# Optimization experiments

Hardware: AMD Instinct MI355X
Metric: run time of the kernel (lower is better)

The kernel has to match this reference:

```python
import jax, jax.numpy as jnp
import numpy as np


def _elem_mlp(x, w1, b1, w2, b2):
    # elementwise 1 -> N -> 1 ReLU MLP (distilled exp / inv approximators)
    h = jax.nn.relu(x[..., None] * w1[:, 0] + b1)  # [..., N]
    return jnp.einsum('...n,n->...', h, w2[0]) + b2[0]


def setup_inputs() -> dict:
    key = jax.random.key(0)
    ks = jax.random.split(key, 13)
    T, S, B, D = 8, 512, 8, 512
    NE, NI = 32, 64
    f = jnp.float32
    inp = {
        'sx': jax.random.normal(ks[0], (T, S, B, D), f) * 0.1,
        'q_proj_weight': jax.random.normal(ks[1], (D, D), f) / np.sqrt(D),
        'k_proj_weight': jax.random.normal(ks[2], (D, D), f) / np.sqrt(D),
        'q_proj_bias': jax.random.normal(ks[3], (D,), f) * 0.02,
        'k_proj_bias': jax.random.normal(ks[4], (D,), f) * 0.02,
        'exp_w1': jax.random.normal(ks[5], (NE, 1), f),
        'exp_b1': jax.random.normal(ks[6], (NE,), f) * 0.1,
        'exp_w2': jax.random.normal(ks[7], (1, NE), f) / np.sqrt(NE),
        'exp_b2': jax.random.normal(ks[8], (1,), f) * 0.01,
        'inv_w1': jax.random.normal(ks[9], (NI, 1), f),
        'inv_b1': jax.random.normal(ks[10], (NI,), f) * 0.1,
        'inv_w2': jax.random.normal(ks[11], (1, NI), f) / np.sqrt(NI),
        'inv_b2': jax.random.normal(ks[12], (1,), f) * 0.01,
        'num_heads': 8,
    }
    return inp


def reference(sx, q_proj_weight, k_proj_weight, q_proj_bias, k_proj_bias,
              exp_w1, exp_b1, exp_w2, exp_b2,
              inv_w1, inv_b1, inv_w2, inv_b2, num_heads):
    T, S, B, D = sx.shape
    H = num_heads
    hd = D // H
    scale = 1.0 / np.sqrt(hd)

    def proj(x_t, W, b):
        # [S, B, D] -> [B*H, S, hd]
        y = x_t @ W.T + b
        return y.reshape(S, B * H, hd).transpose(1, 0, 2)

    def step(carry, x_t):
        sum_q, sum_k, sum_p = carry
        sq = proj(x_t, q_proj_weight, q_proj_bias)
        sk = proj(x_t, k_proj_weight, k_proj_bias)
        sum_q = sum_q + sq
        # sp_t = sum_q @ sk^T + sq @ sum_k^T (sum_k updated AFTER, per snn_qk_product)
        sp = (jnp.einsum('bsh,bth->bst', sum_q, sk)
              + jnp.einsum('bsh,bth->bst', sq, sum_k)) * scale
        sum_k = sum_k + sk
        return (sum_q, sum_k, sum_p + sp), None

    z_qk = jnp.zeros((B * H, S, hd), sx.dtype)
    z_p = jnp.zeros((B * H, S, S), sx.dtype)
    (sum_q, sum_k, sum_p), _ = jax.lax.scan(step, (z_qk, z_qk, z_p), sx)

    p = sum_p / T  # time-averaged accumulated QK product

    # fit_softmax: distilled-MLP softmax approximation
    tmax = p[:, :, 0:1]
    tp = jnp.minimum(p - (tmax - 1.0), 3.0)
    x_up = jnp.where(tp > -20.0,
                     _elem_mlp(tp, exp_w1, exp_b1, exp_w2, exp_b2), 0.0)
    partition = x_up.sum(-1, keepdims=True)
    p_inv = _elem_mlp(partition, inv_w1, inv_b1, inv_w2, inv_b2)
    out = x_up * p_inv
    partition_p2 = out.sum(-1, keepdims=True)
    p_inv2 = _elem_mlp(partition_p2, inv_w1, inv_b1, inv_w2, inv_b2)
    out2 = jnp.where(partition_p2 > 1.5, out * p_inv2, out)
    return out2
```

## Files before the change

### kernel.cpp

```cpp
#include <hip/hip_runtime.h>


#define T_  8
#define NE_ 32
#define NI_ 64

#define LUT_N   4096
#define LUT_LO  -20.0f
#define LUT_HI  3.0f
#define LUT_INVW (LUT_N / (LUT_HI - LUT_LO))
#define LUT_W    ((LUT_HI - LUT_LO) / LUT_N)

typedef __attribute__((ext_vector_type(8))) short bf16x8;
typedef __attribute__((ext_vector_type(4))) float f32x4;

#define XS_OFF 0u
#define WQ_OFF 2097152u
#define WK_OFF 2359296u
#define QB_OFF 2621440u
#define KB_OFF 4718592u
#define LUT_OFF 6815744u

__device__ inline unsigned short f2bf(float f) {
  union { float f; unsigned u; } v; v.f = f;
  unsigned r = v.u + 0x7FFFu + ((v.u >> 16) & 1u);
  return (unsigned short)(r >> 16);
}

__device__ inline void gload16(const void* g, void* l) {
  __builtin_amdgcn_global_load_lds(
      (const __attribute__((address_space(1))) void*)g,
      (__attribute__((address_space(3))) void*)l, 16, 0, 0);
}

__device__ inline bf16x8 lds_read_swz(const unsigned short* base, int row, int byteoff) {
  int addr = row * 128 + (byteoff ^ ((row & 7) << 4));
  return *(const bf16x8*)((const char*)base + addr);
}

__device__ inline float invmlp(float x, const float* __restrict__ w1,
                               const float* __restrict__ b1,
                               const float* __restrict__ w2, float b2) {
  float a = b2;
#pragma unroll 8
  for (int n = 0; n < NI_; n++) a += w2[n] * fmaxf(x * w1[n] + b1[n], 0.0f);
  return a;
}

__device__ inline float expmlp_exact(float t, const float* __restrict__ w1,
                                     const float* __restrict__ b1,
                                     const float* __restrict__ w2, float b2) {
  float a = b2;
#pragma unroll
  for (int n = 0; n < NE_; n++) a += w2[n] * fmaxf(t * w1[n] + b1[n], 0.0f);
  return a;
}

__global__ __launch_bounds__(256) void k_pre(
    const float* __restrict__ sx, const float* __restrict__ wq,
    const float* __restrict__ wk, const float* __restrict__ ew1,
    const float* __restrict__ eb1, const float* __restrict__ ew2,
    const float* __restrict__ eb2p,
    unsigned short* __restrict__ xs, unsigned short* __restrict__ wqb,
    unsigned short* __restrict__ wkb, float2* __restrict__ lut) {
  int bx = blockIdx.x, tid = threadIdx.x;
  if (bx < 2048) {
    size_t i = ((size_t)bx * 256 + tid) * 4;
    float4 a = *(const float4*)(sx + i);
#pragma unroll
    for (int t = 1; t < T_; t++) {
      float4 v = *(const float4*)(sx + (size_t)t * 2097152 + i);
      a.x += v.x; a.y += v.y; a.z += v.z; a.w += v.w;
    }
    ushort4 o; o.x = f2bf(a.x); o.y = f2bf(a.y); o.z = f2bf(a.z); o.w = f2bf(a.w);
    *(ushort4*)(xs + i) = o;
  } else if (bx < 2560) {
    const float* src = (bx < 2304) ? wq : wk;
    unsigned short* dst = (bx < 2304) ? wqb : wkb;
    int base = (bx < 2304) ? 2048 : 2304;
    size_t i = ((size_t)(bx - base) * 256 + tid) * 4;
    float4 a = *(const float4*)(src + i);
    ushort4 o; o.x = f2bf(a.x); o.y = f2bf(a.y); o.z = f2bf(a.z); o.w = f2bf(a.w);
    *(ushort4*)(dst + i) = o;
  } else {
    int i = (bx - 2560) * 256 + tid;
    float b2 = eb2p[0];
    float tl = fmaf((float)i, LUT_W, LUT_LO);
    float th = fmaf((float)(i + 1), LUT_W, LUT_LO);
    float el = expmlp_exact(tl, ew1, eb1, ew2, b2);
    float eh = expmlp_exact(th, ew1, eb1, ew2, b2);
    float alpha = (eh - el) * LUT_INVW;
    float beta = fmaf(-alpha, tl, el);
    lut[i] = make_float2(alpha, beta);
  }
}

__global__ __launch_bounds__(256, 2) void k_proj(
    const unsigned short* __restrict__ xs, const unsigned short* __restrict__ wb,
    const float* __restrict__ bq, const float* __restrict__ bk,
    unsigned short* __restrict__ outb) {
  __shared__ unsigned short As[128 * 64];
  __shared__ unsigned short Bs[128 * 64];
  int tid = threadIdx.x;
  int lane = tid & 63, w = tid >> 6;
  int r0 = blockIdx.x * 128;
  int c0 = blockIdx.y * 128;
  int z = blockIdx.z;
  const unsigned short* W = wb + (size_t)z * 262144;
  const float* bias = z ? bk : bq;
  unsigned short* dst = outb + (size_t)z * 2097152;
  float sc = z ? 1.0f : (1.0f / 64.0f);

  int rgrp = lane >> 4, cl = lane & 15;
  int r0w = (w >> 1) * 64, c0w = (w & 1) * 64;

  f32x4 acc[4][4];
  f32x4 zero = {0.f, 0.f, 0.f, 0.f};
#pragma unroll
  for (int m = 0; m < 4; m++)
#pragma unroll
    for (int n = 0; n < 4; n++) acc[m][n] = zero;

  int rl = lane >> 3, slot = lane & 7;

  for (int kt = 0; kt < 8; kt++) {
    int k0 = kt * 64;
#pragma unroll
    for (int i = 0; i < 4; i++) {
      int chunk = w * 4 + i;
      int r = chunk * 8 + rl;
      int sw = (slot ^ (r & 7)) * 8;
      gload16(xs + (size_t)(r0 + r) * 512 + k0 + sw, (char*)As + chunk * 1024);
      gload16(W + (size_t)(c0 + r) * 512 + k0 + sw, (char*)Bs + chunk * 1024);
    }
    __syncthreads();
#pragma unroll
    for (int kb = 0; kb < 2; kb++) {
      bf16x8 af[4], bfr[4];
#pragma unroll
      for (int m = 0; m < 4; m++) af[m] = lds_read_swz(As, r0w + 16 * m + cl, kb * 64 + rgrp * 16);
#pragma unroll
      for (int n = 0; n < 4; n++) bfr[n] = lds_read_swz(Bs, c0w + 16 * n + cl, kb * 64 + rgrp * 16);
#pragma unroll
      for (int m = 0; m < 4; m++)
#pragma unroll
        for (int n = 0; n < 4; n++)
          acc[m][n] = __builtin_amdgcn_mfma_f32_16x16x32_bf16(af[m], bfr[n], acc[m][n], 0, 0, 0);
    }
    __syncthreads();
  }

#pragma unroll
  for (int n = 0; n < 4; n++) {
    int cg = c0 + c0w + 16 * n + cl;
    float bv = 8.0f * bias[cg];
    int h = cg >> 6, dh = cg & 63;
    int chunk = dh >> 3, hh = chunk >> 2, rg2 = chunk & 3, jj = dh & 7;
#pragma unroll
    for (int m = 0; m < 4; m++) {
#pragma unroll
      for (int j = 0; j < 4; j++) {
        int rg = r0 + r0w + 16 * m + rgrp * 4 + j;
        int s = rg >> 3, b = rg & 7;
        int bh = b * 8 + h;
        int cb = s >> 4, cls = s & 15;
        size_t idx = ((size_t)((bh * 32 + cb) * 2 + hh)) * 512 + (rg2 * 16 + cls) * 8 + jj;
        dst[idx] = f2bf((acc[m][n][j] + bv) * sc);
      }
    }
  }
}

__global__ __launch_bounds__(256, 4) void k_attn(
    const unsigned short* __restrict__ qb, const unsigned short* __restrict__ kb,
    const float2* __restrict__ lutg,
    const float* __restrict__ iw1, const float* __restrict__ ib1,
    const float* __restrict__ iw2, const float* __restrict__ ib2p,
    float* __restrict__ out) {
  __shared__ float2 Lut[LUT_N];
  __shared__ float s_part[4][16];
  __shared__ float s_fac[16];

  int tid = threadIdx.x;
  int lane = tid & 63, w = tid >> 6;
  int i = blockIdx.x;
  int xcd = i & 7, j2 = i >> 3;
  int bh = xcd * 8 + (j2 >> 5);
  int rb = j2 & 31;
  int rgrp = lane >> 4, cl = lane & 15;

#pragma unroll
  for (int c = 0; c < 8; c++) {
    int chunk = w * 8 + c;
    gload16((const char*)lutg + chunk * 1024 + lane * 16, (char*)Lut + chunk * 1024);
  }

  const char* Qb = (const char*)qb + (size_t)((bh * 32 + rb) * 2) * 1024;
  bf16x8 aF0 = *(const bf16x8*)(Qb + lane * 16);
  bf16x8 aF1 = *(const bf16x8*)(Qb + 1024 + lane * 16);

  const char* Kbase = (const char*)kb + (size_t)(bh * 32) * 2048;
  f32x4 zero = {0.f, 0.f, 0.f, 0.f};

  float tm1[4];
  {
    bf16x8 b0 = *(const bf16x8*)(Kbase + lane * 16);
    bf16x8 b1 = *(const bf16x8*)(Kbase + 1024 + lane * 16);
    f32x4 p0 = __builtin_amdgcn_mfma_f32_16x16x32_bf16(aF0, b0, zero, 0, 0, 0);
    p0 = __builtin_amdgcn_mfma_f32_16x16x32_bf16(aF1, b1, p0, 0, 0, 0);
    int src = lane & 48;
#pragma unroll
    for (int j = 0; j < 4; j++) tm1[j] = __shfl(p0[j], src) - 1.0f;
  }

  f32x4 acc[8];
#pragma unroll
  for (int f = 0; f < 8; f++) {
    const char* Kb = Kbase + (size_t)(w * 8 + f) * 2048;
    bf16x8 b0 = *(const bf16x8*)(Kb + lane * 16);
    bf16x8 b1 = *(const bf16x8*)(Kb + 1024 + lane * 16);
    acc[f] = __builtin_amdgcn_mfma_f32_16x16x32_bf16(aF0, b0, zero, 0, 0, 0);
    acc[f] = __builtin_amdgcn_mfma_f32_16x16x32_bf16(aF1, b1, acc[f], 0, 0, 0);
  }

  __syncthreads();

  const float C0 = -LUT_LO * LUT_INVW;
  float rowsum[4] = {0.f, 0.f, 0.f, 0.f};
#pragma unroll
  for (int f = 0; f < 8; f++) {
#pragma unroll
    for (int j = 0; j < 4; j++) {
      float tp = fminf(acc[f][j] - tm1[j], 3.0f);
      float u = fmaf(tp, LUT_INVW, C0);
      u = fminf(fmaxf(u, 0.0f), (float)(LUT_N - 1));
      float2 ab = Lut[(int)u];
      float xu = fmaf(ab.x, tp, ab.y);
      xu = (tp > -20.0f) ? xu : 0.0f;
      acc[f][j] = xu;
      rowsum[j] += xu;
    }
  }

#pragma unroll
  for (int j = 0; j < 4; j++) {
    float s = rowsum[j];
    s += __shfl_xor(s, 1);
    s += __shfl_xor(s, 2);
    s += __shfl_xor(s, 4);
    s += __shfl_xor(s, 8);
    if (cl == 0) s_part[w][rgrp * 4 + j] = s;
  }
  __syncthreads();

  if (tid < 16) {
    float part = s_part[0][tid] + s_part[1][tid] + s_part[2][tid] + s_part[3][tid];
    float pinv = invmlp(part, iw1, ib1, iw2, ib2p[0]);
    float pp2 = part * pinv;
    float fac = pinv;
    if (pp2 > 1.5f) fac *= invmlp(pp2, iw1, ib1, iw2, ib2p[0]);
    s_fac[tid] = fac;
  }
  __syncthreads();

  float* outb = out + ((size_t)bh * 512 + rb * 16) * 512;
#pragma unroll
  for (int j = 0; j < 4; j++) {
    int row = rgrp * 4 + j;
    float fac = s_fac[row];
#pragma unroll
    for (int f = 0; f < 8; f++)
      __builtin_nontemporal_store(acc[f][j] * fac,
          &outb[(size_t)row * 512 + w * 128 + 16 * f + cl]);
  }
}

extern "C" void kernel_launch(void* const* d_in, const int* in_sizes, int n_in,
                              void* d_out, int out_size, void* d_ws, size_t ws_size,
                              hipStream_t stream) {
  (void)in_sizes; (void)n_in; (void)out_size; (void)ws_size;
  const float* sx  = (const float*)d_in[0];
  const float* wq  = (const float*)d_in[1];
  const float* wk  = (const float*)d_in[2];
  const float* bq  = (const float*)d_in[3];
  const float* bk  = (const float*)d_in[4];
  const float* ew1 = (const float*)d_in[5];
  const float* eb1 = (const float*)d_in[6];
  const float* ew2 = (const float*)d_in[7];
  const float* eb2 = (const float*)d_in[8];
  const float* iw1 = (const float*)d_in[9];
  const float* ib1 = (const float*)d_in[10];
  const float* iw2 = (const float*)d_in[11];
  const float* ib2 = (const float*)d_in[12];
  unsigned short* wsu = (unsigned short*)d_ws;
  float2* lut = (float2*)(wsu + LUT_OFF);
  float* out = (float*)d_out;

  k_pre<<<2576, 256, 0, stream>>>(sx, wq, wk, ew1, eb1, ew2, eb2,
                                  wsu + XS_OFF, wsu + WQ_OFF, wsu + WK_OFF, lut);
  k_proj<<<dim3(32, 4, 2), 256, 0, stream>>>(wsu + XS_OFF, wsu + WQ_OFF, bq, bk, wsu + QB_OFF);
  k_attn<<<2048, 256, 0, stream>>>(wsu + QB_OFF, wsu + KB_OFF, lut,
                                   iw1, ib1, iw2, ib2, out);
}
```

Measured before the change: 55.47 us.

## Stage projection output in LDS, shrink LUT to values, parallelize inverse MLP

The projection epilogue now writes its bf16 results into shared memory and then emits coalesced 16-byte stores, replacing scattered 2-byte global stores. The exp lookup table stores one value per point instead of an (alpha, beta) pair and interpolates between neighbours, which halves its shared memory footprint and allows occupancy 5 for the attention kernel. The inverse MLP is now computed redundantly by every lane with four accumulators and broadcast by shuffle, which removes a barrier and the single-wavefront serial section. The input time-sum uses nontemporal loads. Costs are two LDS reads per lookup and duplicated MLP work on every lane.

```diff
diff --git a/kernel.cpp b/kernel.cpp
--- a/kernel.cpp
+++ b/kernel.cpp
@@ -13,6 +13,7 @@
 
 typedef __attribute__((ext_vector_type(8))) short bf16x8;
 typedef __attribute__((ext_vector_type(4))) float f32x4;
+typedef __attribute__((ext_vector_type(4))) unsigned int u32x4;
 
 #define XS_OFF 0u
 #define WQ_OFF 2097152u
@@ -38,13 +39,18 @@
   return *(const bf16x8*)((const char*)base + addr);
 }
 
-__device__ inline float invmlp(float x, const float* __restrict__ w1,
-                               const float* __restrict__ b1,
-                               const float* __restrict__ w2, float b2) {
-  float a = b2;
-#pragma unroll 8
-  for (int n = 0; n < NI_; n++) a += w2[n] * fmaxf(x * w1[n] + b1[n], 0.0f);
-  return a;
+__device__ inline float invmlp4(float x, const float* __restrict__ w1,
+                                const float* __restrict__ b1,
+                                const float* __restrict__ w2, float b2) {
+  float a0 = b2, a1 = 0.f, a2 = 0.f, a3 = 0.f;
+#pragma unroll
+  for (int n = 0; n < NI_; n += 4) {
+    a0 += w2[n + 0] * fmaxf(x * w1[n + 0] + b1[n + 0], 0.0f);
+    a1 += w2[n + 1] * fmaxf(x * w1[n + 1] + b1[n + 1], 0.0f);
+    a2 += w2[n + 2] * fmaxf(x * w1[n + 2] + b1[n + 2], 0.0f);
+    a3 += w2[n + 3] * fmaxf(x * w1[n + 3] + b1[n + 3], 0.0f);
+  }
+  return (a0 + a1) + (a2 + a3);
 }
 
 __device__ inline float expmlp_exact(float t, const float* __restrict__ w1,
@@ -62,17 +68,17 @@
     const float* __restrict__ eb1, const float* __restrict__ ew2,
     const float* __restrict__ eb2p,
     unsigned short* __restrict__ xs, unsigned short* __restrict__ wqb,
-    unsigned short* __restrict__ wkb, float2* __restrict__ lut) {
+    unsigned short* __restrict__ wkb, float* __restrict__ lut) {
   int bx = blockIdx.x, tid = threadIdx.x;
   if (bx < 2048) {
     size_t i = ((size_t)bx * 256 + tid) * 4;
-    float4 a = *(const float4*)(sx + i);
+    f32x4 a = __builtin_nontemporal_load((const f32x4*)(sx + i));
 #pragma unroll
     for (int t = 1; t < T_; t++) {
-      float4 v = *(const float4*)(sx + (size_t)t * 2097152 + i);
-      a.x += v.x; a.y += v.y; a.z += v.z; a.w += v.w;
-    }
-    ushort4 o; o.x = f2bf(a.x); o.y = f2bf(a.y); o.z = f2bf(a.z); o.w = f2bf(a.w);
+      f32x4 v = __builtin_nontemporal_load((const f32x4*)(sx + (size_t)t * 2097152 + i));
+      a += v;
+    }
+    ushort4 o; o.x = f2bf(a[0]); o.y = f2bf(a[1]); o.z = f2bf(a[2]); o.w = f2bf(a[3]);
     *(ushort4*)(xs + i) = o;
   } else if (bx < 2560) {
     const float* src = (bx < 2304) ? wq : wk;
@@ -84,14 +90,10 @@
     *(ushort4*)(dst + i) = o;
   } else {
     int i = (bx - 2560) * 256 + tid;
-    float b2 = eb2p[0];
-    float tl = fmaf((float)i, LUT_W, LUT_LO);
-    float th = fmaf((float)(i + 1), LUT_W, LUT_LO);
-    float el = expmlp_exact(tl, ew1, eb1, ew2, b2);
-    float eh = expmlp_exact(th, ew1, eb1, ew2, b2);
-    float alpha = (eh - el) * LUT_INVW;
-    float beta = fmaf(-alpha, tl, el);
-    lut[i] = make_float2(alpha, beta);
+    if (i <= LUT_N) {
+      float t = fmaf((float)i, LUT_W, LUT_LO);
+      lut[i] = expmlp_exact(t, ew1, eb1, ew2, eb2p[0]);
+    }
   }
 }
 
@@ -99,8 +101,7 @@
     const unsigned short* __restrict__ xs, const unsigned short* __restrict__ wb,
     const float* __restrict__ bq, const float* __restrict__ bk,
     unsigned short* __restrict__ outb) {
-  __shared__ unsigned short As[128 * 64];
-  __shared__ unsigned short Bs[128 * 64];
+  __shared__ unsigned short Sh[2][128 * 64];
   int tid = threadIdx.x;
   int lane = tid & 63, w = tid >> 6;
   int r0 = blockIdx.x * 128;
@@ -130,17 +131,17 @@
       int chunk = w * 4 + i;
       int r = chunk * 8 + rl;
       int sw = (slot ^ (r & 7)) * 8;
-      gload16(xs + (size_t)(r0 + r) * 512 + k0 + sw, (char*)As + chunk * 1024);
-      gload16(W + (size_t)(c0 + r) * 512 + k0 + sw, (char*)Bs + chunk * 1024);
+      gload16(xs + (size_t)(r0 + r) * 512 + k0 + sw, (char*)Sh[0] + chunk * 1024);
+      gload16(W + (size_t)(c0 + r) * 512 + k0 + sw, (char*)Sh[1] + chunk * 1024);
     }
     __syncthreads();
 #pragma unroll
     for (int kb = 0; kb < 2; kb++) {
       bf16x8 af[4], bfr[4];
 #pragma unroll
-      for (int m = 0; m < 4; m++) af[m] = lds_read_swz(As, r0w + 16 * m + cl, kb * 64 + rgrp * 16);
-#pragma unroll
-      for (int n = 0; n < 4; n++) bfr[n] = lds_read_swz(Bs, c0w + 16 * n + cl, kb * 64 + rgrp * 16);
+      for (int m = 0; m < 4; m++) af[m] = lds_read_swz(Sh[0], r0w + 16 * m + cl, kb * 64 + rgrp * 16);
+#pragma unroll
+      for (int n = 0; n < 4; n++) bfr[n] = lds_read_swz(Sh[1], c0w + 16 * n + cl, kb * 64 + rgrp * 16);
 #pragma unroll
       for (int m = 0; m < 4; m++)
 #pragma unroll
@@ -150,36 +151,46 @@
     __syncthreads();
   }
 
+  unsigned short* Os = &Sh[0][0];
 #pragma unroll
   for (int n = 0; n < 4; n++) {
-    int cg = c0 + c0w + 16 * n + cl;
-    float bv = 8.0f * bias[cg];
-    int h = cg >> 6, dh = cg & 63;
-    int chunk = dh >> 3, hh = chunk >> 2, rg2 = chunk & 3, jj = dh & 7;
+    int cgl = c0w + 16 * n + cl;
+    float bv = 8.0f * bias[c0 + cgl];
+    int h = cgl >> 6, dh = cgl & 63;
+    int hh = dh >> 5, rg2 = (dh >> 3) & 3, jj = dh & 7;
 #pragma unroll
     for (int m = 0; m < 4; m++) {
 #pragma unroll
       for (int j = 0; j < 4; j++) {
-        int rg = r0 + r0w + 16 * m + rgrp * 4 + j;
-        int s = rg >> 3, b = rg & 7;
-        int bh = b * 8 + h;
-        int cb = s >> 4, cls = s & 15;
-        size_t idx = ((size_t)((bh * 32 + cb) * 2 + hh)) * 512 + (rg2 * 16 + cls) * 8 + jj;
-        dst[idx] = f2bf((acc[m][n][j] + bv) * sc);
+        int rgl = r0w + 16 * m + rgrp * 4 + j;
+        int sl = rgl >> 3, b = rgl & 7;
+        Os[(((b * 2 + h) * 2 + hh) * 512) + (rg2 * 16 + sl) * 8 + jj] =
+            f2bf((acc[m][n][j] + bv) * sc);
       }
     }
   }
-}
-
-__global__ __launch_bounds__(256, 4) void k_attn(
+  __syncthreads();
+
+  int cb = r0 >> 7;
+  int h0 = c0 >> 6;
+#pragma unroll
+  for (int i = 0; i < 8; i++) {
+    int unit = i * 256 + tid;
+    int b = unit >> 8, h = (unit >> 7) & 1, hh = (unit >> 6) & 1, inner = unit & 63;
+    int bh = b * 8 + h0 + h;
+    size_t du = ((size_t)((bh * 32 + cb) * 2 + hh)) * 512 + inner * 8;
+    *(u32x4*)(dst + du) = *(const u32x4*)(Os + unit * 8);
+  }
+}
+
+__global__ __launch_bounds__(256, 5) void k_attn(
     const unsigned short* __restrict__ qb, const unsigned short* __restrict__ kb,
-    const float2* __restrict__ lutg,
+    const float* __restrict__ lutg,
     const float* __restrict__ iw1, const float* __restrict__ ib1,
     const float* __restrict__ iw2, const float* __restrict__ ib2p,
     float* __restrict__ out) {
-  __shared__ float2 Lut[LUT_N];
+  __shared__ float Lut[LUT_N + 8];
   __shared__ float s_part[4][16];
-  __shared__ float s_fac[16];
 
   int tid = threadIdx.x;
   int lane = tid & 63, w = tid >> 6;
@@ -190,10 +201,11 @@
   int rgrp = lane >> 4, cl = lane & 15;
 
 #pragma unroll
-  for (int c = 0; c < 8; c++) {
-    int chunk = w * 8 + c;
+  for (int c = 0; c < 4; c++) {
+    int chunk = w * 4 + c;
     gload16((const char*)lutg + chunk * 1024 + lane * 16, (char*)Lut + chunk * 1024);
   }
+  if (tid == 0) Lut[LUT_N] = lutg[LUT_N];
 
   const char* Qb = (const char*)qb + (size_t)((bh * 32 + rb) * 2) * 1024;
   bf16x8 aF0 = *(const bf16x8*)(Qb + lane * 16);
@@ -232,10 +244,11 @@
 #pragma unroll
     for (int j = 0; j < 4; j++) {
       float tp = fminf(acc[f][j] - tm1[j], 3.0f);
-      float u = fmaf(tp, LUT_INVW, C0);
-      u = fminf(fmaxf(u, 0.0f), (float)(LUT_N - 1));
-      float2 ab = Lut[(int)u];
-      float xu = fmaf(ab.x, tp, ab.y);
+      float u = fmaxf(fmaf(tp, LUT_INVW, C0), 0.0f);
+      int bi = (int)fminf(u, (float)(LUT_N - 1));
+      float frac = u - (float)bi;
+      float f0 = Lut[bi], f1 = Lut[bi + 1];
+      float xu = fmaf(frac, f1 - f0, f0);
       xu = (tp > -20.0f) ? xu : 0.0f;
       acc[f][j] = xu;
       rowsum[j] += xu;
@@ -253,24 +266,25 @@
   }
   __syncthreads();
 
-  if (tid < 16) {
-    float part = s_part[0][tid] + s_part[1][tid] + s_part[2][tid] + s_part[3][tid];
-    float pinv = invmlp(part, iw1, ib1, iw2, ib2p[0]);
-    float pp2 = part * pinv;
-    float fac = pinv;
-    if (pp2 > 1.5f) fac *= invmlp(pp2, iw1, ib1, iw2, ib2p[0]);
-    s_fac[tid] = fac;
-  }
-  __syncthreads();
+  float fac;
+  {
+    int myrow = lane & 15;
+    float part = s_part[0][myrow] + s_part[1][myrow] +
+                 s_part[2][myrow] + s_part[3][myrow];
+    float b2 = ib2p[0];
+    fac = invmlp4(part, iw1, ib1, iw2, b2);
+    float pp2 = part * fac;
+    if (pp2 > 1.5f) fac *= invmlp4(pp2, iw1, ib1, iw2, b2);
+  }
 
   float* outb = out + ((size_t)bh * 512 + rb * 16) * 512;
 #pragma unroll
   for (int j = 0; j < 4; j++) {
     int row = rgrp * 4 + j;
-    float fac = s_fac[row];
+    float fj = __shfl(fac, (lane & 48) | row);
 #pragma unroll
     for (int f = 0; f < 8; f++)
-      __builtin_nontemporal_store(acc[f][j] * fac,
+      __builtin_nontemporal_store(acc[f][j] * fj,
           &outb[(size_t)row * 512 + w * 128 + 16 * f + cl]);
   }
 }
@@ -293,10 +307,10 @@
   const float* iw2 = (const float*)d_in[11];
   const float* ib2 = (const float*)d_in[12];
   unsigned short* wsu = (unsigned short*)d_ws;
-  float2* lut = (float2*)(wsu + LUT_OFF);
+  float* lut = (float*)(wsu + LUT_OFF);
   float* out = (float*)d_out;
 
-  k_pre<<<2576, 256, 0, stream>>>(sx, wq, wk, ew1, eb1, ew2, eb2,
+  k_pre<<<2577, 256, 0, stream>>>(sx, wq, wk, ew1, eb1, ew2, eb2,
                                   wsu + XS_OFF, wsu + WQ_OFF, wsu + WK_OFF, lut);
   k_proj<<<dim3(32, 4, 2), 256, 0, stream>>>(wsu + XS_OFF, wsu + WQ_OFF, bq, bk, wsu + QB_OFF);
   k_attn<<<2048, 256, 0, stream>>>(wsu + QB_OFF, wsu + KB_OFF, lut,
```

After: 86.75 us. 1.56x slower.
